# Performance work log

Measured on AMD Instinct MI355X. Metric: run time of the kernel, lower is better.

## Reference

```python
import math
import jax, jax.numpy as jnp
import numpy as np

NEG = -1e6

B, QN, SN, TN, D = 8, 512, 64, 128, 128


def _topk_mask_softmax(scores, k):
    # keep top-k along last axis, set the rest to -1e6, then softmax (matches
    # torch full_like(-1e6).scatter(topk).softmax)
    vals, idx = jax.lax.top_k(scores, k)
    masked = jnp.full_like(scores, NEG)
    masked = jnp.put_along_axis(masked, idx, vals, axis=-1, inplace=False)
    return jax.nn.softmax(masked, axis=-1)


def setup_inputs() -> dict:
    key = jax.random.key(0)
    ks = jax.random.split(key, 11)
    sc = 0.05
    return {
        "queries": jax.random.normal(ks[0], (B, QN, D), jnp.float32),
        "stat_keys": jax.random.normal(ks[1], (B, SN, D), jnp.float32),
        "token_keys": jax.random.normal(ks[2], (B * SN, TN, D), jnp.float32),
        "values": jax.random.normal(ks[3], (B * SN, TN, D), jnp.float32),
        "stat_valid_lens": jax.random.randint(ks[4], (B,), 1, SN + 1),
        "Wq_stat": jax.random.normal(ks[5], (D, D), jnp.float32) * sc,
        "Wq_token": jax.random.normal(ks[6], (D, D), jnp.float32) * sc,
        "Wk_stat": jax.random.normal(ks[7], (D, D), jnp.float32) * sc,
        "Wk_token": jax.random.normal(ks[8], (D, D), jnp.float32) * sc,
        "Wv": jax.random.normal(ks[9], (D, D), jnp.float32) * sc,
        "Wo": jax.random.normal(ks[10], (D, D), jnp.float32) * sc,
        "stat_k": 8,
        "token_k": 16,
    }


def reference(queries, stat_keys, token_keys, values, stat_valid_lens,
              Wq_stat, Wq_token, Wk_stat, Wk_token, Wv, Wo, stat_k, token_k):
    q_stat = queries @ Wq_stat            # [b,q,d]
    q_tok = queries @ Wq_token            # [b,q,d]
    k_stat = stat_keys @ Wk_stat          # [b,s,d]
    k_tok = token_keys @ Wk_token         # [b*s,t,d]
    v = values @ Wv                       # [b*s,t,d]
    b, qn, d = q_stat.shape
    s = k_stat.shape[1]
    t = k_tok.shape[1]
    scale = 1.0 / math.sqrt(d)

    # --- stat level ---
    stat_scores = jnp.einsum('bqd,bsd->bqs', q_stat, k_stat) * scale
    valid = jnp.arange(s)[None, None, :] < stat_valid_lens[:, None, None]
    stat_scores = jnp.where(valid, stat_scores, NEG)
    stat_w = _topk_mask_softmax(stat_scores, min(s - 1, stat_k))  # [b,q,s]

    # --- token level (query_token repeated per stat block) ---
    tok_scores = jnp.einsum('bqd,bstd->bsqt', q_tok, k_tok.reshape(b, s, t, d)) * scale
    tok_w = _topk_mask_softmax(tok_scores, min(t - 1, token_k))   # [b,s,q,t]
    tok_w = tok_w.transpose(0, 2, 1, 3)                           # [b,q,s,t]

    combine = (stat_w[..., None] * tok_w).reshape(b, qn, s * t)   # [b,q,s*t]
    out = jnp.einsum('bqn,bnd->bqd', combine, v.reshape(b, s * t, d))
    return out @ Wo
```

## Files before the change

kernel.cpp:

```cpp
#include <hip/hip_runtime.h>
#include <hip/hip_bf16.h>
#include <math.h>

#define BB 8
#define QN 512
#define SN 64
#define TN 128
#define DD 128
#define STAT_K 8
#define TOK_K 16
#define SCALE 0.08838834764831845f
#define NEGBIG -1e6f
#define NINF  -3.4e38f

typedef float f4 __attribute__((ext_vector_type(4)));
typedef float f2 __attribute__((ext_vector_type(2)));
typedef unsigned long long u64;

__device__ __forceinline__ void proj_tile4_lds(const float* __restrict__ A,
                                               const float* __restrict__ W,
                                               float* __restrict__ C,
                                               int rowBase, int transposed,
                                               int tid, float* __restrict__ wsh)
{
    const int tx = tid & 15;
    const int ty = tid >> 4;
    const float* Ab = A + (size_t)(rowBase + ty * 4) * 128;

    float acc[4][8];
    #pragma unroll
    for (int i = 0; i < 4; ++i)
        #pragma unroll
        for (int j = 0; j < 8; ++j) acc[i][j] = 0.f;

    for (int h = 0; h < 2; ++h) {
        const f4* src = (const f4*)(W + (size_t)h * 64 * 128);
        __syncthreads();
        #pragma unroll
        for (int i2 = 0; i2 < 8; ++i2)
            ((f4*)wsh)[i2 * 256 + tid] = src[i2 * 256 + tid];
        __syncthreads();

        #pragma unroll 2
        for (int k0 = 0; k0 < 64; k0 += 4) {
            f4 a[4];
            #pragma unroll
            for (int i = 0; i < 4; ++i)
                a[i] = *(const f4*)(Ab + i * 128 + h * 64 + k0);
            f4 wl[4], wh[4];
            #pragma unroll
            for (int kk = 0; kk < 4; ++kk) {
                wl[kk] = *(const f4*)&wsh[(k0 + kk) * 128 + tx * 4];
                wh[kk] = *(const f4*)&wsh[(k0 + kk) * 128 + 64 + tx * 4];
            }
            #pragma unroll
            for (int i = 0; i < 4; ++i)
                #pragma unroll
                for (int kk = 0; kk < 4; ++kk)
                    #pragma unroll
                    for (int j = 0; j < 4; ++j) {
                        acc[i][j]     = fmaf(a[i][kk], wl[kk][j], acc[i][j]);
                        acc[i][4 + j] = fmaf(a[i][kk], wh[kk][j], acc[i][4 + j]);
                    }
        }
    }

    if (!transposed) {
        #pragma unroll
        for (int i = 0; i < 4; ++i) {
            size_t row = (size_t)rowBase + ty * 4 + i;
            f4 lo = {acc[i][0], acc[i][1], acc[i][2], acc[i][3]};
            f4 hi = {acc[i][4], acc[i][5], acc[i][6], acc[i][7]};
            *(f4*)&C[row * 128 + tx * 4]      = lo;
            *(f4*)&C[row * 128 + 64 + tx * 4] = hi;
        }
    } else {
        float* Cb = C + ((size_t)(rowBase >> 7) << 14);
        const int rb = (rowBase & 127) + ty * 4;
        #pragma unroll
        for (int j = 0; j < 4; ++j) {
            int clo = tx * 4 + j;
            int chi = 64 + tx * 4 + j;
            f4 v0 = {acc[0][j], acc[1][j], acc[2][j], acc[3][j]};
            f4 v1 = {acc[0][4 + j], acc[1][4 + j], acc[2][4 + j], acc[3][4 + j]};
            *(f4*)&Cb[clo * 128 + rb] = v0;
            *(f4*)&Cb[chi * 128 + rb] = v1;
        }
    }
}

__global__ __launch_bounds__(256) void proj_all(const float* __restrict__ queries,
                                                const float* __restrict__ stat_keys,
                                                const float* __restrict__ token_keys,
                                                const float* __restrict__ Wq_stat,
                                                const float* __restrict__ Wq_token,
                                                const float* __restrict__ Wk_stat,
                                                const float* __restrict__ Wk_token,
                                                const float* __restrict__ Wv,
                                                const float* __restrict__ Wo,
                                                float* __restrict__ q_stat,
                                                float* __restrict__ q_tok,
                                                float* __restrict__ k_stat,
                                                float* __restrict__ kT,
                                                float* __restrict__ M_vo,
                                                int* __restrict__ cnt)
{
    __shared__ float wsh[64 * 128];
    const int bi = blockIdx.x;
    if (bi < 1024)       proj_tile4_lds(token_keys, Wk_token, kT,     bi * 64,           1, threadIdx.x, wsh);
    else if (bi < 1088)  proj_tile4_lds(queries,    Wq_stat,  q_stat, (bi - 1024) * 64,  0, threadIdx.x, wsh);
    else if (bi < 1152)  proj_tile4_lds(queries,    Wq_token, q_tok,  (bi - 1088) * 64,  0, threadIdx.x, wsh);
    else if (bi < 1160)  proj_tile4_lds(stat_keys,  Wk_stat,  k_stat, (bi - 1152) * 64,  0, threadIdx.x, wsh);
    else if (bi < 1162)  proj_tile4_lds(Wv,         Wo,       M_vo,   (bi - 1160) * 64,  0, threadIdx.x, wsh);
    else {
        for (int i = threadIdx.x; i < BB * SN; i += 256) cnt[i] = 0;
    }
}

__global__ __launch_bounds__(64, 4) void stat_topk(const float* __restrict__ qs,
                                                   const float* __restrict__ ks,
                                                   const int* __restrict__ vlen,
                                                   int* __restrict__ sel_i,
                                                   float* __restrict__ sel_w,
                                                   int* __restrict__ cnt,
                                                   int* __restrict__ list,
                                                   float* __restrict__ pvw)
{
    const int bq   = blockIdx.x;
    const int b    = bq >> 9;
    const int lane = threadIdx.x;

    const f4* q4 = (const f4*)(qs + (size_t)bq * 128);
    const f4* k4 = (const f4*)(ks + (size_t)(b * SN + lane) * 128);
    float acc = 0.f;
    #pragma unroll 8
    for (int kk = 0; kk < 32; ++kk) {
        f4 q = q4[kk];
        f4 k = k4[kk];
        acc = fmaf(q[0], k[0], acc);
        acc = fmaf(q[1], k[1], acc);
        acc = fmaf(q[2], k[2], acc);
        acc = fmaf(q[3], k[3], acc);
    }
    float score = acc * SCALE;
    if (lane >= vlen[b]) score = NEGBIG;

    float work = score;
    float tv[STAT_K];
    int   ti[STAT_K];
    #pragma unroll
    for (int j = 0; j < STAT_K; ++j) {
        float m = work;
        #pragma unroll
        for (int off = 32; off > 0; off >>= 1) m = fmaxf(m, __shfl_xor(m, off));
        unsigned long long ball = __ballot(work == m);
        int L = __ffsll(ball) - 1;
        tv[j] = m;
        ti[j] = L;
        if (lane == L) work = NINF;
    }

    float w[STAT_K];
    float Z = 0.f;
    #pragma unroll
    for (int j = 0; j < STAT_K; ++j) { w[j] = expf(tv[j] - tv[0]); Z += w[j]; }
    float invZ = 1.f / Z;

    if (lane < STAT_K) {
        float wv = w[lane] * invZ;
        int pid = bq * STAT_K + lane;
        sel_i[pid] = ti[lane];
        sel_w[pid] = wv;
        if (wv != 0.f) {
            int s  = ti[lane];
            int bs = b * SN + s;
            int pos = atomicAdd(&cnt[bs], 1);
            list[bs * 512 + pos] = (bq & 511) | (lane << 16);
        } else {
            #pragma unroll
            for (int j = 0; j < TOK_K; ++j)
                pvw[(size_t)pid * TOK_K + j] = 0.f;
        }
    }
}

__global__ __launch_bounds__(512) void tok_score_sel(const float* __restrict__ qt,
                                                     const float* __restrict__ kT,
                                                     const int* __restrict__ cnt,
                                                     const int* __restrict__ list,
                                                     const float* __restrict__ sel_w,
                                                     int* __restrict__ pvt,
                                                     float* __restrict__ pvw)
{
    const int bin   = blockIdx.x & 511;
    const int chunk = blockIdx.x >> 9;
    const int b  = bin & 7;
    const int s  = bin >> 3;
    const int bs = b * SN + s;
    const int nq = cnt[bs];
    const int q0 = chunk * 128;
    if (q0 >= nq) return;

    const int tid  = threadIdx.x;
    const int tx   = tid & 15;
    const int ty   = tid >> 4;
    const int lane = tid & 63;
    const int g    = lane >> 4;

    int pid[4];
    float swp[4];
    const float* Ab[4];
    #pragma unroll
    for (int i = 0; i < 4; ++i) {
        int e  = list[bs * 512 + min(q0 + ty * 4 + i, nq - 1)];
        int q  = e & 0xffff;
        int si = (e >> 16) & 7;
        pid[i] = ((b << 9) + q) * 8 + si;
        swp[i] = sel_w[pid[i]];
        Ab[i]  = qt + ((size_t)(b << 9) + q) * 128;
    }
    const float* kb = kT + ((size_t)bs << 14);

    __shared__ float ksh[64 * 128];

    float acc[4][8];
    #pragma unroll
    for (int i = 0; i < 4; ++i)
        #pragma unroll
        for (int j = 0; j < 8; ++j) acc[i][j] = 0.f;

    for (int h = 0; h < 2; ++h) {
        const f4* src = (const f4*)(kb + (size_t)h * 64 * 128);
        __syncthreads();
        #pragma unroll
        for (int it2 = 0; it2 < 4; ++it2)
            ((f4*)ksh)[it2 * 512 + tid] = src[it2 * 512 + tid];
        __syncthreads();

        #pragma unroll 2
        for (int k0 = 0; k0 < 64; k0 += 4) {
            f4 a[4];
            #pragma unroll
            for (int i = 0; i < 4; ++i)
                a[i] = *(const f4*)(Ab[i] + h * 64 + k0);
            f4 wl[4], wh[4];
            #pragma unroll
            for (int kk = 0; kk < 4; ++kk) {
                wl[kk] = *(const f4*)&ksh[(k0 + kk) * 128 + tx * 4];
                wh[kk] = *(const f4*)&ksh[(k0 + kk) * 128 + 64 + tx * 4];
            }
            #pragma unroll
            for (int i = 0; i < 4; ++i)
                #pragma unroll
                for (int kk = 0; kk < 4; ++kk)
                    #pragma unroll
                    for (int j = 0; j < 4; ++j) {
                        acc[i][j]     = fmaf(a[i][kk], wl[kk][j], acc[i][j]);
                        acc[i][4 + j] = fmaf(a[i][kk], wh[kk][j], acc[i][4 + j]);
                    }
        }
    }

    float s8[4][8];
    #pragma unroll
    for (int i = 0; i < 4; ++i)
        #pragma unroll
        for (int j = 0; j < 8; ++j) s8[i][j] = acc[i][j] * SCALE;

    float m0[4], myM[4];
    int   myT[4];
    #pragma unroll
    for (int i = 0; i < 4; ++i) { m0[i] = 0.f; myM[i] = 0.f; myT[i] = 0; }

    for (int it = 0; it < 16; ++it) {
        #pragma unroll
        for (int i = 0; i < 4; ++i) {
            float v01 = fmaxf(s8[i][0], s8[i][1]);
            float v23 = fmaxf(s8[i][2], s8[i][3]);
            float v45 = fmaxf(s8[i][4], s8[i][5]);
            float v67 = fmaxf(s8[i][6], s8[i][7]);
            float m = fmaxf(fmaxf(v01, v23), fmaxf(v45, v67));
            #pragma unroll
            for (int off = 8; off > 0; off >>= 1) m = fmaxf(m, __shfl_xor(m, off));

            int jlo = 4, jhi = 4;
            #pragma unroll
            for (int j = 3; j >= 0; --j) jlo = (s8[i][j]     == m) ? j : jlo;
            #pragma unroll
            for (int j = 3; j >= 0; --j) jhi = (s8[i][4 + j] == m) ? j : jhi;

            u64 blo = __ballot(jlo < 4);
            u64 bhi = __ballot(jhi < 4);
            unsigned mlo = (unsigned)((blo >> (g * 16)) & 0xFFFFu);
            unsigned mhi = (unsigned)((bhi >> (g * 16)) & 0xFFFFu);
            bool lo = (mlo != 0);
            unsigned msel = lo ? mlo : mhi;
            int L = __ffs(msel) - 1;
            int jsel = lo ? jlo : jhi;
            int jwin = __shfl(jsel, g * 16 + L);
            int tstar = (lo ? 0 : 64) + 4 * L + jwin;

            m0[i] = (it == 0) ? m : m0[i];
            bool rec = (tx == it);
            myT[i] = rec ? tstar : myT[i];
            myM[i] = rec ? m : myM[i];

            int slot = (lo ? 0 : 4) + jwin;
            bool winlane = (tx == L);
            #pragma unroll
            for (int j = 0; j < 8; ++j)
                s8[i][j] = (winlane && slot == j) ? NINF : s8[i][j];
        }
    }

    #pragma unroll
    for (int i = 0; i < 4; ++i) {
        float myE = expf(myM[i] - m0[i]);
        float Z = myE;
        #pragma unroll
        for (int off = 8; off > 0; off >>= 1) Z += __shfl_xor(Z, off);
        float cs = swp[i] / Z;

        pvt[(size_t)pid[i] * TOK_K + tx] = myT[i];
        pvw[(size_t)pid[i] * TOK_K + tx] = myE * cs;
    }
}

__global__ __launch_bounds__(256) void tok_pv3(const float* __restrict__ values,
                                               const int* __restrict__ sel_i,
                                               const int* __restrict__ pvt,
                                               const float* __restrict__ pvw,
                                               const float* __restrict__ M_vo,
                                               float* __restrict__ out)
{
    const int wid  = threadIdx.x >> 6;
    const int bq   = blockIdx.x * 4 + wid;
    const int lane = threadIdx.x & 63;
    const int b    = bq >> 9;

    float o0 = 0.f, o1 = 0.f;
    #pragma unroll
    for (int si = 0; si < STAT_K; ++si) {
        const int pid = bq * STAT_K + si;
        const int s   = sel_i[pid];
        const float* vb = values + ((size_t)(b * SN + s) << 14);
        const int*   tp = pvt + (size_t)pid * TOK_K;
        const float* wp = pvw + (size_t)pid * TOK_K;
        #pragma unroll
        for (int j = 0; j < TOK_K; ++j) {
            int   t = tp[j] & 127;
            float w = wp[j];
            f2 x = *(const f2*)(vb + (size_t)t * 128 + lane * 2);
            o0 = fmaf(w, x[0], o0);
            o1 = fmaf(w, x[1], o1);
        }
    }

    __shared__ float pre[4][128];
    *(f2*)&pre[wid][lane * 2] = (f2){o0, o1};
    __asm__ __volatile__("" ::: "memory");
    __builtin_amdgcn_wave_barrier();
    __asm__ __volatile__("" ::: "memory");

    float r0 = 0.f, r1 = 0.f;
    #pragma unroll 4
    for (int d = 0; d < 128; ++d) {
        float p = pre[wid][d];
        f2 w = *(const f2*)(M_vo + (size_t)d * 128 + lane * 2);
        r0 = fmaf(p, w[0], r0);
        r1 = fmaf(p, w[1], r1);
    }
    *(f2*)&out[(size_t)bq * 128 + lane * 2] = (f2){r0, r1};
}

extern "C" void kernel_launch(void* const* d_in, const int* in_sizes, int n_in,
                              void* d_out, int out_size, void* d_ws, size_t ws_size,
                              hipStream_t stream)
{
    const float* queries    = (const float*)d_in[0];
    const float* stat_keys  = (const float*)d_in[1];
    const float* token_keys = (const float*)d_in[2];
    const float* values     = (const float*)d_in[3];
    const int*   vlen       = (const int*)d_in[4];
    const float* Wq_stat    = (const float*)d_in[5];
    const float* Wq_token   = (const float*)d_in[6];
    const float* Wk_stat    = (const float*)d_in[7];
    const float* Wk_token   = (const float*)d_in[8];
    const float* Wv         = (const float*)d_in[9];
    const float* Wo         = (const float*)d_in[10];

    char* ws = (char*)d_ws;
    float* q_stat  = (float*)(ws);
    float* q_tok   = (float*)(ws + 2097152);
    float* k_stat  = (float*)(ws + 4194304);
    float* M_vo    = (float*)(ws + 4456448);
    int*   sel_i   = (int*)  (ws + 4521984);
    float* sel_w   = (float*)(ws + 4653056);
    float* kT      = (float*)(ws + 4784128);
    int*   pvt     = (int*)  (ws + 38338560);
    float* pvw     = (float*)(ws + 40435712);
    int*   list    = (int*)  (ws + 42532864);
    int*   cnt     = (int*)  (ws + 43581440);

    proj_all<<<1163, 256, 0, stream>>>(queries, stat_keys, token_keys,
                                       Wq_stat, Wq_token, Wk_stat, Wk_token, Wv, Wo,
                                       q_stat, q_tok, k_stat, kT, M_vo, cnt);

    stat_topk<<<BB * QN, 64, 0, stream>>>(q_stat, k_stat, vlen, sel_i, sel_w,
                                          cnt, list, pvw);

    tok_score_sel<<<2048, 512, 0, stream>>>(q_tok, kT, cnt, list, sel_w, pvt, pvw);

    tok_pv3<<<BB * QN / 4, 256, 0, stream>>>(values, sel_i, pvt, pvw, M_vo,
                                             (float*)d_out);
}
```

Baseline: 171.6 us.

## Fold Wk_token into query projection instead of projecting all token keys

Rather than projecting every token key by Wk_token (a 65536x128x128 GEMM written out transposed), the query is premultiplied by Wk_token^T, and token scores are computed directly against the raw token_keys, which are transposed into LDS on load. This removes the large token-key projection and its 32MB intermediate write and read. The cost is an extra small kernel launch (proj_q2), a single-block transpose of Wk_token, and scalar strided LDS stores in the score kernel that may bank-conflict.

```diff
diff --git a/kernel.cpp b/kernel.cpp
--- a/kernel.cpp
+++ b/kernel.cpp
@@ -20,8 +20,8 @@
 __device__ __forceinline__ void proj_tile4_lds(const float* __restrict__ A,
                                                const float* __restrict__ W,
                                                float* __restrict__ C,
-                                               int rowBase, int transposed,
-                                               int tid, float* __restrict__ wsh)
+                                               int rowBase, int tid,
+                                               float* __restrict__ wsh)
 {
     const int tx = tid & 15;
     const int ty = tid >> 4;
@@ -65,33 +65,18 @@
         }
     }
 
-    if (!transposed) {
-        #pragma unroll
-        for (int i = 0; i < 4; ++i) {
-            size_t row = (size_t)rowBase + ty * 4 + i;
-            f4 lo = {acc[i][0], acc[i][1], acc[i][2], acc[i][3]};
-            f4 hi = {acc[i][4], acc[i][5], acc[i][6], acc[i][7]};
-            *(f4*)&C[row * 128 + tx * 4]      = lo;
-            *(f4*)&C[row * 128 + 64 + tx * 4] = hi;
-        }
-    } else {
-        float* Cb = C + ((size_t)(rowBase >> 7) << 14);
-        const int rb = (rowBase & 127) + ty * 4;
-        #pragma unroll
-        for (int j = 0; j < 4; ++j) {
-            int clo = tx * 4 + j;
-            int chi = 64 + tx * 4 + j;
-            f4 v0 = {acc[0][j], acc[1][j], acc[2][j], acc[3][j]};
-            f4 v1 = {acc[0][4 + j], acc[1][4 + j], acc[2][4 + j], acc[3][4 + j]};
-            *(f4*)&Cb[clo * 128 + rb] = v0;
-            *(f4*)&Cb[chi * 128 + rb] = v1;
-        }
+    #pragma unroll
+    for (int i = 0; i < 4; ++i) {
+        size_t row = (size_t)rowBase + ty * 4 + i;
+        f4 lo = {acc[i][0], acc[i][1], acc[i][2], acc[i][3]};
+        f4 hi = {acc[i][4], acc[i][5], acc[i][6], acc[i][7]};
+        *(f4*)&C[row * 128 + tx * 4]      = lo;
+        *(f4*)&C[row * 128 + 64 + tx * 4] = hi;
     }
 }
 
 __global__ __launch_bounds__(256) void proj_all(const float* __restrict__ queries,
                                                 const float* __restrict__ stat_keys,
-                                                const float* __restrict__ token_keys,
                                                 const float* __restrict__ Wq_stat,
                                                 const float* __restrict__ Wq_token,
                                                 const float* __restrict__ Wk_stat,
@@ -101,20 +86,39 @@
                                                 float* __restrict__ q_stat,
                                                 float* __restrict__ q_tok,
                                                 float* __restrict__ k_stat,
-                                                float* __restrict__ kT,
                                                 float* __restrict__ M_vo,
+                                                float* __restrict__ WkT,
                                                 int* __restrict__ cnt)
 {
     __shared__ float wsh[64 * 128];
     const int bi = blockIdx.x;
-    if (bi < 1024)       proj_tile4_lds(token_keys, Wk_token, kT,     bi * 64,           1, threadIdx.x, wsh);
-    else if (bi < 1088)  proj_tile4_lds(queries,    Wq_stat,  q_stat, (bi - 1024) * 64,  0, threadIdx.x, wsh);
-    else if (bi < 1152)  proj_tile4_lds(queries,    Wq_token, q_tok,  (bi - 1088) * 64,  0, threadIdx.x, wsh);
-    else if (bi < 1160)  proj_tile4_lds(stat_keys,  Wk_stat,  k_stat, (bi - 1152) * 64,  0, threadIdx.x, wsh);
-    else if (bi < 1162)  proj_tile4_lds(Wv,         Wo,       M_vo,   (bi - 1160) * 64,  0, threadIdx.x, wsh);
-    else {
+    if (bi < 64)         proj_tile4_lds(queries,   Wq_stat,  q_stat, bi * 64,        threadIdx.x, wsh);
+    else if (bi < 128)   proj_tile4_lds(queries,   Wq_token, q_tok, (bi - 64) * 64,  threadIdx.x, wsh);
+    else if (bi < 136)   proj_tile4_lds(stat_keys, Wk_stat,  k_stat,(bi - 128) * 64, threadIdx.x, wsh);
+    else if (bi < 138)   proj_tile4_lds(Wv,        Wo,       M_vo,  (bi - 136) * 64, threadIdx.x, wsh);
+    else if (bi == 138) {
+        #pragma unroll
+        for (int i2 = 0; i2 < 16; ++i2) {
+            int idx = i2 * 256 + threadIdx.x;
+            int e  = idx >> 5;
+            int d4 = idx & 31;
+            f4 v = *(const f4*)(Wk_token + (size_t)e * 128 + d4 * 4);
+            WkT[(size_t)(d4 * 4 + 0) * 128 + e] = v[0];
+            WkT[(size_t)(d4 * 4 + 1) * 128 + e] = v[1];
+            WkT[(size_t)(d4 * 4 + 2) * 128 + e] = v[2];
+            WkT[(size_t)(d4 * 4 + 3) * 128 + e] = v[3];
+        }
+    } else {
         for (int i = threadIdx.x; i < BB * SN; i += 256) cnt[i] = 0;
     }
+}
+
+__global__ __launch_bounds__(256) void proj_q2(const float* __restrict__ q_tok,
+                                               const float* __restrict__ WkT,
+                                               float* __restrict__ q2)
+{
+    __shared__ float wsh[64 * 128];
+    proj_tile4_lds(q_tok, WkT, q2, blockIdx.x * 64, threadIdx.x, wsh);
 }
 
 __global__ __launch_bounds__(64, 4) void stat_topk(const float* __restrict__ qs,
@@ -184,8 +188,8 @@
     }
 }
 
-__global__ __launch_bounds__(512) void tok_score_sel(const float* __restrict__ qt,
-                                                     const float* __restrict__ kT,
+__global__ __launch_bounds__(512) void tok_score_sel(const float* __restrict__ q2,
+                                                     const float* __restrict__ token_keys,
                                                      const int* __restrict__ cnt,
                                                      const int* __restrict__ list,
                                                      const float* __restrict__ sel_w,
@@ -217,9 +221,9 @@
         int si = (e >> 16) & 7;
         pid[i] = ((b << 9) + q) * 8 + si;
         swp[i] = sel_w[pid[i]];
-        Ab[i]  = qt + ((size_t)(b << 9) + q) * 128;
-    }
-    const float* kb = kT + ((size_t)bs << 14);
+        Ab[i]  = q2 + ((size_t)(b << 9) + q) * 128;
+    }
+    const float* kb = token_keys + ((size_t)bs << 14);
 
     __shared__ float ksh[64 * 128];
 
@@ -229,12 +233,23 @@
         #pragma unroll
         for (int j = 0; j < 8; ++j) acc[i][j] = 0.f;
 
+    const int st   = tid & 127;
+    const int dgrp = tid >> 7;
+
     for (int h = 0; h < 2; ++h) {
-        const f4* src = (const f4*)(kb + (size_t)h * 64 * 128);
         __syncthreads();
-        #pragma unroll
-        for (int it2 = 0; it2 < 4; ++it2)
-            ((f4*)ksh)[it2 * 512 + tid] = src[it2 * 512 + tid];
+        {
+            const float* src = kb + (size_t)st * 128 + h * 64 + dgrp * 16;
+            #pragma unroll
+            for (int it2 = 0; it2 < 4; ++it2) {
+                f4 v = *(const f4*)(src + it2 * 4);
+                int dc = dgrp * 16 + it2 * 4;
+                ksh[(dc + 0) * 128 + st] = v[0];
+                ksh[(dc + 1) * 128 + st] = v[1];
+                ksh[(dc + 2) * 128 + st] = v[2];
+                ksh[(dc + 3) * 128 + st] = v[3];
+            }
+        }
         __syncthreads();
 
         #pragma unroll 2
@@ -394,22 +409,26 @@
     float* q_tok   = (float*)(ws + 2097152);
     float* k_stat  = (float*)(ws + 4194304);
     float* M_vo    = (float*)(ws + 4456448);
-    int*   sel_i   = (int*)  (ws + 4521984);
-    float* sel_w   = (float*)(ws + 4653056);
-    float* kT      = (float*)(ws + 4784128);
-    int*   pvt     = (int*)  (ws + 38338560);
-    float* pvw     = (float*)(ws + 40435712);
-    int*   list    = (int*)  (ws + 42532864);
-    int*   cnt     = (int*)  (ws + 43581440);
-
-    proj_all<<<1163, 256, 0, stream>>>(queries, stat_keys, token_keys,
-                                       Wq_stat, Wq_token, Wk_stat, Wk_token, Wv, Wo,
-                                       q_stat, q_tok, k_stat, kT, M_vo, cnt);
+    float* WkT     = (float*)(ws + 4521984);
+    int*   sel_i   = (int*)  (ws + 4587520);
+    float* sel_w   = (float*)(ws + 4718592);
+    float* q2      = (float*)(ws + 4849664);
+    int*   pvt     = (int*)  (ws + 6946816);
+    float* pvw     = (float*)(ws + 9043968);
+    int*   list    = (int*)  (ws + 11141120);
+    int*   cnt     = (int*)  (ws + 12189696);
+
+    proj_all<<<140, 256, 0, stream>>>(queries, stat_keys,
+                                      Wq_stat, Wq_token, Wk_stat, Wk_token, Wv, Wo,
+                                      q_stat, q_tok, k_stat, M_vo, WkT, cnt);
+
+    proj_q2<<<64, 256, 0, stream>>>(q_tok, WkT, q2);
 
     stat_topk<<<BB * QN, 64, 0, stream>>>(q_stat, k_stat, vlen, sel_i, sel_w,
                                           cnt, list, pvw);
 
-    tok_score_sel<<<2048, 512, 0, stream>>>(q_tok, kT, cnt, list, sel_w, pvt, pvw);
+    tok_score_sel<<<2048, 512, 0, stream>>>(q2, token_keys, cnt, list, sel_w,
+                                            pvt, pvw);
 
     tok_pv3<<<BB * QN / 4, 256, 0, stream>>>(values, sel_i, pvt, pvw, M_vo,
                                              (float*)d_out);
```

Result: faster. 159.6 us (-6.9%).
